# Kernel tuning notes

Measured on AMD Instinct MI355X. Metric: run time of the kernel, lower is better.

The kernel has to match this reference:

```python
import jax, jax.numpy as jnp
import numpy as np

# Static multi-level feature-map shapes (H, W) per level.
SPATIAL_SHAPES = np.array([[92, 160], [46, 80], [23, 40], [12, 20]], dtype=np.int32)
NUM_HEADS = 8
NUM_LEVELS = 4
NUM_POINTS = 4      # sampling points per head per level (num_all_points)
NUM_Z = 4           # num_Z_anchors; NUM_POINTS % NUM_Z == 0
EMBED = 256
HEAD_DIM = EMBED // NUM_HEADS


def setup_inputs() -> dict:
    key = jax.random.key(0)
    ks = jax.random.split(key, 10)
    bs, nq = 2, 10000
    nv = int((SPATIAL_SHAPES[:, 0] * SPATIAL_SHAPES[:, 1]).sum())  # 19560
    query = jax.random.normal(ks[0], (bs, nq, EMBED), jnp.float32)
    value = jax.random.normal(ks[1], (bs, nv, EMBED), jnp.float32)
    query_pos = jax.random.normal(ks[2], (bs, nq, EMBED), jnp.float32)
    reference_points = jax.random.uniform(ks[3], (bs, nq, NUM_Z, 2), jnp.float32)
    W_val = jax.random.normal(ks[4], (EMBED, EMBED), jnp.float32) / jnp.sqrt(EMBED)
    b_val = jnp.zeros((EMBED,), jnp.float32)
    W_off = jax.random.normal(ks[5], (EMBED, NUM_HEADS * NUM_LEVELS * NUM_POINTS * 2), jnp.float32) * 0.01
    b_off = jax.random.normal(ks[6], (NUM_HEADS * NUM_LEVELS * NUM_POINTS * 2,), jnp.float32) * 0.5
    W_attn = jax.random.normal(ks[7], (EMBED, NUM_HEADS * NUM_LEVELS * NUM_POINTS), jnp.float32) * 0.02
    b_attn = jnp.zeros((NUM_HEADS * NUM_LEVELS * NUM_POINTS,), jnp.float32)
    spatial_shapes = jnp.asarray(SPATIAL_SHAPES)
    return {
        'query': query, 'value': value, 'query_pos': query_pos,
        'reference_points': reference_points,
        'W_val': W_val, 'b_val': b_val, 'W_off': W_off, 'b_off': b_off,
        'W_attn': W_attn, 'b_attn': b_attn, 'spatial_shapes': spatial_shapes,
    }


def _bilinear(v, x, y, H, W):
    """grid_sample(mode='bilinear', padding_mode='zeros', align_corners=False).

    v: (bs, H, W, heads, d); x, y: (bs, nq, heads, P) pixel coords.
    Returns (bs, nq, heads, P, d).
    """
    x0 = jnp.floor(x)
    y0 = jnp.floor(y)
    wx1 = x - x0
    wy1 = y - y0
    wx0 = 1.0 - wx1
    wy0 = 1.0 - wy1
    x0i = x0.astype(jnp.int32)
    y0i = y0.astype(jnp.int32)
    b = jnp.arange(v.shape[0])[:, None, None, None]
    h = jnp.arange(v.shape[3])[None, None, :, None]

    def gather(yi, xi):
        valid = (yi >= 0) & (yi < H) & (xi >= 0) & (xi < W)
        yc = jnp.clip(yi, 0, H - 1)
        xc = jnp.clip(xi, 0, W - 1)
        g = v[b, yc, xc, h]  # (bs, nq, heads, P, d)
        return g * valid[..., None].astype(v.dtype)

    return (gather(y0i, x0i) * (wy0 * wx0)[..., None]
            + gather(y0i, x0i + 1) * (wy0 * wx1)[..., None]
            + gather(y0i + 1, x0i) * (wy1 * wx0)[..., None]
            + gather(y0i + 1, x0i + 1) * (wy1 * wx1)[..., None])


def reference(query, value, query_pos, reference_points, W_val, b_val,
              W_off, b_off, W_attn, b_attn, spatial_shapes):
    bs, nq, _ = query.shape
    q = query + query_pos
    # value projection -> per-head values
    v = (value @ W_val + b_val).reshape(bs, -1, NUM_HEADS, HEAD_DIM)
    # sampling offsets and attention weights from query
    off = (q @ W_off + b_off).reshape(bs, nq, NUM_HEADS, NUM_LEVELS, NUM_POINTS, 2)
    attn = (q @ W_attn + b_attn).reshape(bs, nq, NUM_HEADS, NUM_LEVELS * NUM_POINTS)
    attn = jax.nn.softmax(attn, axis=-1).reshape(bs, nq, NUM_HEADS, NUM_LEVELS, NUM_POINTS)
    # normalize offsets by (w, h) of each level
    norm = jnp.stack([spatial_shapes[:, 1], spatial_shapes[:, 0]], -1).astype(q.dtype)  # (L, 2)
    off = off / norm[None, None, None, :, None, :]
    # fold Z-anchor reference points in, matching the shape[-1]==2 branch
    off = off.reshape(bs, nq, NUM_HEADS, NUM_LEVELS, NUM_POINTS // NUM_Z, NUM_Z, 2)
    loc = reference_points[:, :, None, None, None, :, :] + off
    loc = loc.reshape(bs, nq, NUM_HEADS, NUM_LEVELS, NUM_POINTS, 2)
    grid = 2.0 * loc - 1.0  # grid_sample convention

    start = 0
    sampled = []
    for lvl in range(NUM_LEVELS):
        H, W = int(SPATIAL_SHAPES[lvl, 0]), int(SPATIAL_SHAPES[lvl, 1])
        vl = v[:, start:start + H * W].reshape(bs, H, W, NUM_HEADS, HEAD_DIM)
        start += H * W
        # align_corners=False pixel coords
        x = ((grid[:, :, :, lvl, :, 0] + 1.0) * W - 1.0) * 0.5
        y = ((grid[:, :, :, lvl, :, 1] + 1.0) * H - 1.0) * 0.5
        sampled.append(_bilinear(vl, x, y, H, W))
    samp = jnp.stack(sampled, axis=3)  # (bs, nq, heads, L, P, d)
    out = (samp * attn[..., None]).sum(axis=(3, 4))  # (bs, nq, heads, d)
    return out.reshape(bs, nq, NUM_HEADS * HEAD_DIM)
```

## Files before the change

kernel.cpp:

```cpp
#include <hip/hip_runtime.h>

#define NQ 10000
#define BS 2
#define NV 19560
#define NH 8
#define HD 32
#define EMB 256

typedef __attribute__((ext_vector_type(8))) short bf16x8;
typedef __attribute__((ext_vector_type(4))) float f32x4;
typedef __attribute__((ext_vector_type(4))) short s16x4;

__device__ __forceinline__ unsigned short f2bf(float x) {
    unsigned u = __float_as_uint(x);
    u += 0x7FFFu + ((u >> 16) & 1u);
    return (unsigned short)(u >> 16);
}

__global__ __launch_bounds__(256) void convert_W(
    const float* __restrict__ Wv, const float* __restrict__ Wo,
    const float* __restrict__ Wa, const float* __restrict__ bv,
    const float* __restrict__ bo, const float* __restrict__ ba,
    ushort* __restrict__ Bt, float* __restrict__ bias) {
    int n = blockIdx.x;
    int k = threadIdx.x;
    float x;
    if (n < 256)       x = Wv[k * 256 + n];
    else if (n < 512)  x = Wo[k * 256 + (n - 256)];
    else               x = Wa[k * 128 + (n - 512)];
    Bt[n * 256 + k] = f2bf(x);
    if (k == 0)
        bias[n] = (n < 256) ? bv[n] : (n < 512) ? bo[n - 256] : ba[n - 512];
}

__global__ __launch_bounds__(256) void gemm_fused(
    const float* __restrict__ value, const float* __restrict__ query,
    const float* __restrict__ qpos, const ushort* __restrict__ Bt,
    const float* __restrict__ bias,
    ushort* __restrict__ Cv, float* __restrict__ C0, float* __restrict__ C1)
{
    __shared__ short As[64][40], Bhs[128][40];

    const int tid = threadIdx.x;

    const int bid0 = blockIdx.x;
    int bid;
    if (bid0 < 1224) {
        bid = (bid0 & 7) * 153 + (bid0 >> 3);
    } else {
        int q = bid0 - 1224;
        int xcd = q & 7, idx = q >> 3;
        int orig = (xcd < 3) ? (xcd * 118 + idx)
                             : (3 * 118 + (xcd - 3) * 117 + idx);
        bid = 1224 + orig;
    }

    bool isval; int mblk, npan;
    if (bid < 1224) { isval = true;  mblk = bid >> 1; npan = bid & 1; }
    else { int q = bid - 1224; isval = false; mblk = q / 3; npan = q % 3; }

    const int M  = isval ? (BS * NV) : (BS * NQ);
    const int m0 = mblk * 64;
    const int n0 = npan * 128;
    const int nbase = (isval ? 0 : 256) + n0;

    const float* A = isval ? value : query;

    const int arow = tid >> 2;
    const int acol = (tid & 3) * 8;
    const bool aval = (m0 + arow) < M;
    const float* Ap  = A    + (size_t)(m0 + arow) * 256 + acol;
    const float* A2p = qpos + (size_t)(m0 + arow) * 256 + acol;
    const int brow = tid >> 1;
    const int bcol = (tid & 1) * 16;
    const ushort* Bp = Bt + (size_t)(nbase + brow) * 256 + bcol;

    const int lane = tid & 63, wave = tid >> 6;
    const int wrow = (wave >> 1) * 32, wcol = (wave & 1) * 64;
    const int lr = lane & 15, quad = lane >> 4, lk = quad * 8;

    f32x4 acc[2][4] = {};

    for (int k0 = 0; k0 < 256; k0 += 32) {
        #pragma unroll
        for (int g = 0; g < 2; g++) {
            f32x4 v = {};
            if (aval) {
                v = *(const f32x4*)(Ap + k0 + g * 4);
                if (!isval) v += *(const f32x4*)(A2p + k0 + g * 4);
            }
            s16x4 hh;
            #pragma unroll
            for (int e = 0; e < 4; e++) hh[e] = (short)f2bf(v[e]);
            *(s16x4*)&As[arow][acol + g * 4] = hh;
        }
        *(bf16x8*)&Bhs[brow][bcol]     = *(const bf16x8*)(Bp + k0);
        *(bf16x8*)&Bhs[brow][bcol + 8] = *(const bf16x8*)(Bp + k0 + 8);
        __syncthreads();

        bf16x8 af[2], bhf[4];
        #pragma unroll
        for (int i = 0; i < 2; i++)
            af[i] = *(const bf16x8*)&As[wrow + i * 16 + lr][lk];
        #pragma unroll
        for (int j = 0; j < 4; j++)
            bhf[j] = *(const bf16x8*)&Bhs[wcol + j * 16 + lr][lk];
        #pragma unroll
        for (int i = 0; i < 2; i++)
            #pragma unroll
            for (int j = 0; j < 4; j++)
                acc[i][j] = __builtin_amdgcn_mfma_f32_16x16x32_bf16(af[i], bhf[j], acc[i][j], 0, 0, 0);
        __syncthreads();
    }

    #pragma unroll
    for (int j = 0; j < 4; j++) {
        int cc = wcol + j * 16 + lr;
        int col = n0 + cc;
        float bb = bias[nbase + cc];
        #pragma unroll
        for (int i = 0; i < 2; i++) {
            int gmb = m0 + wrow + i * 16 + quad * 4;
            #pragma unroll
            for (int r = 0; r < 4; r++) {
                int gm = gmb + r;
                if (gm < M) {
                    float val = acc[i][j][r] + bb;
                    if (isval) {
                        int h = col >> 5, d = col & 31;
                        int b = (gm >= NV) ? 1 : 0;
                        int pix = gm - b * NV;
                        Cv[((size_t)(b * 8 + h) * NV + pix) * 32 + d] = f2bf(val);
                    } else {
                        if (col < 256) C0[(size_t)gm * 256 + col] = val;
                        else           C1[(size_t)gm * 128 + (col - 256)] = val;
                    }
                }
            }
        }
    }
}

__global__ __launch_bounds__(256) void sample4(
    const ushort* __restrict__ v, const float* __restrict__ off,
    const float* __restrict__ attn, const float* __restrict__ refp,
    float* __restrict__ out)
{
    __shared__ int   s_off[256][5];
    __shared__ float s_w[256][5];

    const int bq0 = blockIdx.x * 2;
    const int t = threadIdx.x;

    {
        const int bq = bq0 + (t >> 7);
        const int b = (bq >= NQ) ? 1 : 0;
        const int i = t & 127;
        const int h = i >> 4, l = (i >> 2) & 3, p = i & 3;

        float logit = attn[(size_t)bq * 128 + i];
        float mx = logit;
        #pragma unroll
        for (int m = 1; m < 16; m <<= 1) mx = fmaxf(mx, __shfl_xor(mx, m, 16));
        float e = __expf(logit - mx);
        float s = e;
        #pragma unroll
        for (int m = 1; m < 16; m <<= 1) s += __shfl_xor(s, m, 16);
        float w = e / s;

        const float Wf[4] = {160.f, 80.f, 40.f, 20.f};
        const float Hf[4] = {92.f, 46.f, 23.f, 12.f};
        const int   Wi[4] = {160, 80, 40, 20};
        const int   Hi[4] = {92, 46, 23, 12};
        const int   st[4] = {0, 14720, 18400, 19320};

        float ox = off[(size_t)bq * 256 + h * 32 + l * 8 + p * 2];
        float oy = off[(size_t)bq * 256 + h * 32 + l * 8 + p * 2 + 1];
        float rx = refp[(size_t)bq * 8 + p * 2];
        float ry = refp[(size_t)bq * 8 + p * 2 + 1];
        float x = rx * Wf[l] + ox - 0.5f;
        float y = ry * Hf[l] + oy - 0.5f;
        float x0f = floorf(x), y0f = floorf(y);
        float wx1 = x - x0f, wy1 = y - y0f;
        float wx0 = 1.f - wx1, wy0 = 1.f - wy1;
        int x0 = (int)x0f, y0 = (int)y0f;
        const int W = Wi[l], H = Hi[l];
        float mx0 = ((unsigned)x0       < (unsigned)W) ? 1.f : 0.f;
        float mx1 = ((unsigned)(x0 + 1) < (unsigned)W) ? 1.f : 0.f;
        float my0 = ((unsigned)y0       < (unsigned)H) ? 1.f : 0.f;
        float my1 = ((unsigned)(y0 + 1) < (unsigned)H) ? 1.f : 0.f;
        int xc0 = min(max(x0, 0), W - 1);
        int xc1 = min(max(x0 + 1, 0), W - 1);
        int yc0 = min(max(y0, 0), H - 1);
        int yc1 = min(max(y0 + 1, 0), H - 1);
        int base = ((b * 8 + h) * NV + st[l]) * 32;
        s_off[t][0] = base + (yc0 * W + xc0) * 32;
        s_off[t][1] = base + (yc0 * W + xc1) * 32;
        s_off[t][2] = base + (yc1 * W + xc0) * 32;
        s_off[t][3] = base + (yc1 * W + xc1) * 32;
        s_w[t][0] = w * wy0 * wx0 * my0 * mx0;
        s_w[t][1] = w * wy0 * wx1 * my0 * mx1;
        s_w[t][2] = w * wy1 * wx0 * my1 * mx0;
        s_w[t][3] = w * wy1 * wx1 * my1 * mx1;
    }
    __syncthreads();

    const int g = t >> 4;
    const int lane = t & 15;
    const int qi = g >> 3, h = g & 7;
    const int bq = bq0 + qi;
    const int d2 = lane * 2;
    const int pbase = qi * 128 + h * 16;

    float acc0 = 0.f, acc1 = 0.f, acc2 = 0.f, acc3 = 0.f;
    #pragma unroll
    for (int ib = 0; ib < 4; ib++) {
        int o[16]; float wgt[16];
        #pragma unroll
        for (int pp = 0; pp < 4; pp++) {
            int idx = pbase + ib * 4 + pp;
            #pragma unroll
            for (int c = 0; c < 4; c++) {
                o[pp * 4 + c]   = s_off[idx][c];
                wgt[pp * 4 + c] = s_w[idx][c];
            }
        }
        unsigned u[16];
        #pragma unroll
        for (int j = 0; j < 16; j++)
            u[j] = *(const unsigned*)(v + o[j] + d2);
        #pragma unroll
        for (int j = 0; j < 16; j += 2) {
            acc0 += wgt[j]     * __uint_as_float(u[j] << 16);
            acc1 += wgt[j]     * __uint_as_float(u[j] & 0xffff0000u);
            acc2 += wgt[j + 1] * __uint_as_float(u[j + 1] << 16);
            acc3 += wgt[j + 1] * __uint_as_float(u[j + 1] & 0xffff0000u);
        }
    }
    float2 res = make_float2(acc0 + acc2, acc1 + acc3);
    *(float2*)(out + (size_t)bq * 256 + h * 32 + d2) = res;
}

extern "C" void kernel_launch(void* const* d_in, const int* in_sizes, int n_in,
                              void* d_out, int out_size, void* d_ws, size_t ws_size,
                              hipStream_t stream) {
    const float* query     = (const float*)d_in[0];
    const float* value     = (const float*)d_in[1];
    const float* query_pos = (const float*)d_in[2];
    const float* refp      = (const float*)d_in[3];
    const float* W_val     = (const float*)d_in[4];
    const float* b_val     = (const float*)d_in[5];
    const float* W_off     = (const float*)d_in[6];
    const float* b_off     = (const float*)d_in[7];
    const float* W_attn    = (const float*)d_in[8];
    const float* b_attn    = (const float*)d_in[9];
    float* out = (float*)d_out;

    char* w = (char*)d_ws;
    float*  off    = (float*)w;   w += 20480000;
    float*  attn   = (float*)w;   w += 10240000;
    ushort* vp_bf  = (ushort*)w;  w += 20029440;
    ushort* Bt     = (ushort*)w;  w += 327680;
    float*  bias_c = (float*)w;   w += 2560;

    convert_W<<<640, 256, 0, stream>>>(W_val, W_off, W_attn, b_val, b_off, b_attn,
                                       Bt, bias_c);

    gemm_fused<<<1224 + 939, 256, 0, stream>>>(value, query, query_pos, Bt, bias_c,
                                               vp_bf, off, attn);

    sample4<<<BS * NQ / 2, 256, 0, stream>>>(vp_bf, off, attn, refp, out);
}
```

Measured before the change: 214.3 us.

## Remap sampling blocks to one batch-head pair over sixteen queries

Each sampling block now handles a single (batch, head) pair for 16 consecutive queries, where it previously handled two queries across all heads. Within a block, gathers then all read the head-major value plane of one head, which is meant to improve L2 locality of the bilinear gathers. Block indices are interleaved so that consecutive blocks cycle through the 16 batch-head combinations. In exchange, reads of offsets, attention logits and output writes become strided per head, and the reference points are reloaded once per head.

```diff
diff --git a/kernel.cpp b/kernel.cpp
--- a/kernel.cpp
+++ b/kernel.cpp
@@ -149,16 +149,19 @@
     __shared__ int   s_off[256][5];
     __shared__ float s_w[256][5];
 
-    const int bq0 = blockIdx.x * 2;
     const int t = threadIdx.x;
+    const int combo = blockIdx.x & 15;
+    const int qgrp  = blockIdx.x >> 4;
+    const int b  = combo & 1;
+    const int h0 = combo >> 1;
 
     {
-        const int bq = bq0 + (t >> 7);
-        const int b = (bq >= NQ) ? 1 : 0;
-        const int i = t & 127;
-        const int h = i >> 4, l = (i >> 2) & 3, p = i & 3;
-
-        float logit = attn[(size_t)bq * 128 + i];
+        const int qloc = t >> 4;
+        const int lp   = t & 15;
+        const int l = lp >> 2, p = lp & 3;
+        const size_t bq = (size_t)b * NQ + qgrp * 16 + qloc;
+
+        float logit = attn[bq * 128 + h0 * 16 + lp];
         float mx = logit;
         #pragma unroll
         for (int m = 1; m < 16; m <<= 1) mx = fmaxf(mx, __shfl_xor(mx, m, 16));
@@ -174,10 +177,10 @@
         const int   Hi[4] = {92, 46, 23, 12};
         const int   st[4] = {0, 14720, 18400, 19320};
 
-        float ox = off[(size_t)bq * 256 + h * 32 + l * 8 + p * 2];
-        float oy = off[(size_t)bq * 256 + h * 32 + l * 8 + p * 2 + 1];
-        float rx = refp[(size_t)bq * 8 + p * 2];
-        float ry = refp[(size_t)bq * 8 + p * 2 + 1];
+        float ox = off[bq * 256 + h0 * 32 + l * 8 + p * 2];
+        float oy = off[bq * 256 + h0 * 32 + l * 8 + p * 2 + 1];
+        float rx = refp[bq * 8 + p * 2];
+        float ry = refp[bq * 8 + p * 2 + 1];
         float x = rx * Wf[l] + ox - 0.5f;
         float y = ry * Hf[l] + oy - 0.5f;
         float x0f = floorf(x), y0f = floorf(y);
@@ -193,7 +196,7 @@
         int xc1 = min(max(x0 + 1, 0), W - 1);
         int yc0 = min(max(y0, 0), H - 1);
         int yc1 = min(max(y0 + 1, 0), H - 1);
-        int base = ((b * 8 + h) * NV + st[l]) * 32;
+        int base = ((b * 8 + h0) * NV + st[l]) * 32;
         s_off[t][0] = base + (yc0 * W + xc0) * 32;
         s_off[t][1] = base + (yc0 * W + xc1) * 32;
         s_off[t][2] = base + (yc1 * W + xc0) * 32;
@@ -207,10 +210,9 @@
 
     const int g = t >> 4;
     const int lane = t & 15;
-    const int qi = g >> 3, h = g & 7;
-    const int bq = bq0 + qi;
+    const size_t bq = (size_t)b * NQ + qgrp * 16 + g;
     const int d2 = lane * 2;
-    const int pbase = qi * 128 + h * 16;
+    const int pbase = g * 16;
 
     float acc0 = 0.f, acc1 = 0.f, acc2 = 0.f, acc3 = 0.f;
     #pragma unroll
@@ -238,7 +240,7 @@
         }
     }
     float2 res = make_float2(acc0 + acc2, acc1 + acc3);
-    *(float2*)(out + (size_t)bq * 256 + h * 32 + d2) = res;
+    *(float2*)(out + bq * 256 + h0 * 32 + d2) = res;
 }
 
 extern "C" void kernel_launch(void* const* d_in, const int* in_sizes, int n_in,
@@ -269,5 +271,5 @@
     gemm_fused<<<1224 + 939, 256, 0, stream>>>(value, query, query_pos, Bt, bias_c,
                                                vp_bf, off, attn);
 
-    sample4<<<BS * NQ / 2, 256, 0, stream>>>(vp_bf, off, attn, refp, out);
-}
+    sample4<<<(BS * NQ / 16) * NH, 256, 0, stream>>>(vp_bf, off, attn, refp, out);
+}
```

Measured after the change: 203.6 us, median of 2. 5.0% less time.
